# Kernel tuning notes

Measured on AMD Instinct MI355X. Metric: run time of the kernel, lower is better.

The kernel has to match this reference:

```python
import jax, jax.numpy as jnp
import numpy as np

NUM_BLOCKS, NUM_LAYERS = 3, 10
DILATIONS = tuple(2 ** l for l in range(NUM_LAYERS)) * NUM_BLOCKS  # 30 layers
B, T = 2, 8192
MEL_C, RES_C, SKIP_C, K = 80, 512, 256, 3


def conv1d(x, w, b, dilation=1):
    # x: (B, Cin, T), w: (Cout, Cin, K), 'same' padding = dilation*(K-1)//2
    pad = dilation * (w.shape[-1] - 1) // 2
    y = jax.lax.conv_general_dilated(
        x, w, window_strides=(1,), padding=[(pad, pad)],
        rhs_dilation=(dilation,), dimension_numbers=("NCH", "OIH", "NCH"))
    return y + b[None, :, None]


def setup_inputs() -> dict:
    key = jax.random.key(0)
    ks = jax.random.split(key, 16)
    s = 0.05  # keep activations in a sane range through the gated stack
    return {
        "mel_spec": jax.random.normal(ks[0], (B, MEL_C, T), jnp.float32),
        "audio":    jax.random.normal(ks[1], (B, 1, T), jnp.float32),
        "start_w":  jax.random.normal(ks[2], (RES_C, 1, 1), jnp.float32) * s,
        "start_b":  jax.random.normal(ks[3], (RES_C,), jnp.float32) * s,
        "mel_w":    jax.random.normal(ks[4], (RES_C, MEL_C, 1), jnp.float32) * s,
        "mel_b":    jax.random.normal(ks[5], (RES_C,), jnp.float32) * s,
        "dil_w":    jax.random.normal(ks[6], (30, 2 * RES_C, RES_C, K), jnp.float32) * s,
        "dil_b":    jax.random.normal(ks[7], (30, 2 * RES_C), jnp.float32) * s,
        "res_w":    jax.random.normal(ks[8], (30, RES_C, RES_C, 1), jnp.float32) * s,
        "res_b":    jax.random.normal(ks[9], (30, RES_C), jnp.float32) * s,
        "skip_w":   jax.random.normal(ks[10], (30, SKIP_C, RES_C, 1), jnp.float32) * s,
        "skip_b":   jax.random.normal(ks[11], (30, SKIP_C), jnp.float32) * s,
        "fc1_w":    jax.random.normal(ks[12], (SKIP_C, SKIP_C, 1), jnp.float32) * s,
        "fc1_b":    jax.random.normal(ks[13], (SKIP_C,), jnp.float32) * s,
        "fc2_w":    jax.random.normal(ks[14], (1, SKIP_C, 1), jnp.float32) * s,
        "fc2_b":    jax.random.normal(ks[15], (1,), jnp.float32) * s,
    }


def reference(mel_spec, audio, start_w, start_b, mel_w, mel_b,
              dil_w, dil_b, res_w, res_b, skip_w, skip_b,
              fc1_w, fc1_b, fc2_w, fc2_b):
    x = conv1d(audio, start_w, start_b)                 # (B, RES_C, T)
    mel_cond = conv1d(mel_spec, mel_w, mel_b)           # (B, RES_C, T) -- same length, no interp
    x = x + mel_cond
    skip_sum = jnp.zeros((x.shape[0], SKIP_C, x.shape[2]), x.dtype)
    for i, d in enumerate(DILATIONS):                   # 30 structurally distinct layers
        h = conv1d(x, dil_w[i], dil_b[i], dilation=d)   # (B, 2*RES_C, T)
        f, g = jnp.split(h, 2, axis=1)
        a = jnp.tanh(f) * jax.nn.sigmoid(g)             # gated activation
        x = x + conv1d(a, res_w[i], res_b[i])
        skip_sum = skip_sum + conv1d(a, skip_w[i], skip_b[i])
    y = jax.nn.relu(conv1d(skip_sum, fc1_w, fc1_b))
    return jnp.tanh(conv1d(y, fc2_w, fc2_b))            # (B, 1, T)
```

## Files before the change

### kernel.cpp

```cpp
#include <hip/hip_runtime.h>
#include <stdint.h>

#define TB 8192
#define NBATCH 2
#define RES_C 512
#define SKIP_C 256
#define MEL_C 80
#define NLAYERS 30

typedef short v8s __attribute__((ext_vector_type(8)));
typedef float v4f __attribute__((ext_vector_type(4)));
typedef unsigned short v4u16 __attribute__((ext_vector_type(4)));
typedef unsigned short v8u16 __attribute__((ext_vector_type(8)));

__device__ __forceinline__ unsigned short bf16rne(float f) {
    unsigned u = __float_as_uint(f);
    return (unsigned short)((u + 0x7fffu + ((u >> 16) & 1u)) >> 16);
}
__device__ __forceinline__ float bf2f(unsigned short h) {
    return __uint_as_float((unsigned)h << 16);
}
__device__ __forceinline__ float fsigmoid(float x) { return 1.0f / (1.0f + __expf(-x)); }
__device__ __forceinline__ float ftanh_(float x) { return 2.0f / (1.0f + __expf(-2.0f * x)) - 1.0f; }

__device__ __forceinline__ void gld16(const void* g, void* l) {
    __builtin_amdgcn_global_load_lds(
        (const __attribute__((address_space(1))) unsigned int*)g,
        (__attribute__((address_space(3))) unsigned int*)l, 16, 0, 0);
}

__global__ void k0_pack(const float* __restrict__ dil_w,
                        const float* __restrict__ res_w,
                        const float* __restrict__ skip_w,
                        unsigned short* __restrict__ WdH, unsigned short* __restrict__ WdL,
                        unsigned short* __restrict__ WrH, unsigned short* __restrict__ WrL,
                        unsigned short* __restrict__ WsH, unsigned short* __restrict__ WsL,
                        int split)
{
    const int NWd3 = NLAYERS * 1024 * 512;
    const int NWr = NLAYERS * 512 * 512;
    const int NWs = NLAYERS * 256 * 512;
    const int total = NWd3 + NWr + NWs;
    const int stride = gridDim.x * blockDim.x;
    for (int i = blockIdx.x * blockDim.x + threadIdx.x; i < total; i += stride) {
        if (i < NWd3) {
            const int ci = i & 511;
            int t2 = i >> 9;
            const int co = t2 & 1023;
            const int l = t2 >> 10;
            const float* src = dil_w + (size_t)i * 3;
            #pragma unroll
            for (int tap = 0; tap < 3; ++tap) {
                const float w = src[tap];
                const size_t d = ((size_t)(l * 3 + tap) * 1024 + co) * 512 + ci;
                const unsigned short h = bf16rne(w);
                WdH[d] = h;
                if (split) WdL[d] = bf16rne(w - bf2f(h));
            }
        } else if (i < NWd3 + NWr) {
            const int j2 = i - NWd3;
            const float w = res_w[j2];
            const unsigned short h = bf16rne(w);
            WrH[j2] = h;
            if (split) WrL[j2] = bf16rne(w - bf2f(h));
        } else {
            const int j2 = i - NWd3 - NWr;
            const float w = skip_w[j2];
            const unsigned short h = bf16rne(w);
            WsH[j2] = h;
            if (split) WsL[j2] = bf16rne(w - bf2f(h));
        }
    }
}

__global__ __launch_bounds__(512)
void k_init(const float* __restrict__ audio, const float* __restrict__ mel,
            const float* __restrict__ start_w, const float* __restrict__ start_b,
            const float* __restrict__ mel_w, const float* __restrict__ mel_b,
            float* __restrict__ x0,
            unsigned short* __restrict__ xH, unsigned short* __restrict__ xL,
            float* __restrict__ skip_acc, int split)
{
    __shared__ float smel[MEL_C][64];
    __shared__ float sa[64];
    const int tid = threadIdx.x;
    const int b = blockIdx.x >> 7;
    const int t0 = (blockIdx.x & 127) << 6;
    for (int i = tid; i < MEL_C * 64; i += 512) {
        const int m = i >> 6, tt = i & 63;
        smel[m][tt] = mel[((size_t)b * MEL_C + m) * TB + t0 + tt];
    }
    if (tid < 64) sa[tid] = audio[(size_t)b * TB + t0 + tid];
    for (int i = tid; i < 64 * SKIP_C; i += 512) {
        const int tt = i >> 8, c = i & 255;
        skip_acc[(size_t)(b * TB + t0 + tt) * SKIP_C + c] = 0.f;
    }
    __syncthreads();
    const int c = tid;
    const float sw = start_w[c];
    const float bias = start_b[c] + mel_b[c];
    const float* wrow = mel_w + (size_t)c * MEL_C;
    v4f acc[16];
    #pragma unroll
    for (int q = 0; q < 16; ++q) {
        v4f av = *(const v4f*)&sa[q * 4];
        acc[q][0] = fmaf(sw, av[0], bias);
        acc[q][1] = fmaf(sw, av[1], bias);
        acc[q][2] = fmaf(sw, av[2], bias);
        acc[q][3] = fmaf(sw, av[3], bias);
    }
    for (int m = 0; m < MEL_C; ++m) {
        const float w = wrow[m];
        #pragma unroll
        for (int q = 0; q < 16; ++q) {
            v4f mv = *(const v4f*)&smel[m][q * 4];
            acc[q][0] = fmaf(w, mv[0], acc[q][0]);
            acc[q][1] = fmaf(w, mv[1], acc[q][1]);
            acc[q][2] = fmaf(w, mv[2], acc[q][2]);
            acc[q][3] = fmaf(w, mv[3], acc[q][3]);
        }
    }
    #pragma unroll
    for (int q = 0; q < 16; ++q) {
        #pragma unroll
        for (int e = 0; e < 4; ++e) {
            const int tt = q * 4 + e;
            const size_t o = (size_t)(b * TB + t0 + tt) * RES_C + c;
            const float v = acc[q][e];
            x0[o] = v;
            const unsigned short h = bf16rne(v);
            xH[o] = h;
            if (split) xL[o] = bf16rne(v - bf2f(h));
        }
    }
}

__global__ __launch_bounds__(512)
void k1_dilgate(const unsigned short* __restrict__ xH,
                const unsigned short* __restrict__ xL,
                unsigned short* __restrict__ aH, unsigned short* __restrict__ aL,
                const unsigned short* __restrict__ WdH,
                const unsigned short* __restrict__ WdL,
                const float* __restrict__ dil_b,
                int dil, int split)
{
    __shared__ unsigned short shb2[2][128 * 128];
    __shared__ unsigned short slb2[2][128 * 128];
    const int tid = threadIdx.x;
    const int wave = tid >> 6, lane = tid & 63;
    const int quad = lane >> 4, l15 = lane & 15;
    const int p = blockIdx.x & 1;
    const int tl = blockIdx.x >> 1;
    const int b = tl >> 6;
    const int t0 = (tl & 63) << 7;
    const int fbase = p * 256 + wave * 32;
    const int srow = lane >> 4;
    const int schunk = lane & 15;

    const v4f vz = {0.f, 0.f, 0.f, 0.f};
    v4f accF[2][8], accG[2][8];
    #pragma unroll
    for (int mt = 0; mt < 2; ++mt)
        #pragma unroll
        for (int n = 0; n < 8; ++n) { accF[mt][n] = vz; accG[mt][n] = vz; }

    auto stage = [&](int chunk, int buf) {
        const int tap = chunk >> 2, ks = chunk & 3;
        const int off = (tap - 1) * dil;
        const bool allok = (t0 + off >= 0) && (t0 + 127 + off < TB);
        unsigned short* dsth = shb2[buf];
        unsigned short* dstl = slb2[buf];
        if (allok) {
            #pragma unroll
            for (int q = 0; q < 4; ++q) {
                const int rbase = wave * 16 + q * 4;
                const int r = rbase + srow;
                const size_t go = (size_t)(b * TB + t0 + r + off) * RES_C
                                + ks * 128 + ((schunk ^ (r & 7)) << 3);
                gld16(xH + go, dsth + rbase * 128);
                if (split) gld16(xL + go, dstl + rbase * 128);
            }
        } else {
            #pragma unroll
            for (int q = 0; q < 4; ++q) {
                const int rbase = wave * 16 + q * 4;
                const int r = rbase + srow;
                const int tsrc = t0 + r + off;
                const bool ok = (unsigned)tsrc < TB;
                const size_t go = (size_t)(b * TB + tsrc) * RES_C
                                + ks * 128 + ((schunk ^ (r & 7)) << 3);
                v8u16 vh = ok ? *(const v8u16*)(xH + go) : (v8u16)0;
                *(v8u16*)(dsth + rbase * 128 + (lane << 3)) = vh;
                if (split) {
                    v8u16 vl = ok ? *(const v8u16*)(xL + go) : (v8u16)0;
                    *(v8u16*)(dstl + rbase * 128 + (lane << 3)) = vl;
                }
            }
        }
    };

    auto compute = [&](int chunk, int buf) {
        const int tap = chunk >> 2, ks = chunk & 3;
        const unsigned short* WHT = WdH + (size_t)tap * 1024 * 512;
        const unsigned short* WLT = WdL + (size_t)tap * 1024 * 512;
        const unsigned short* shb = shb2[buf];
        const unsigned short* slb = slb2[buf];
        #pragma unroll
        for (int kc = 0; kc < 4; ++kc) {
            const int kg = ks * 128 + kc * 32 + quad * 8;
            v8s afh[2], agh[2], afl[2], agl[2];
            #pragma unroll
            for (int mt = 0; mt < 2; ++mt) {
                const int row = fbase + mt * 16 + l15;
                afh[mt] = *(const v8s*)(WHT + (size_t)row * 512 + kg);
                agh[mt] = *(const v8s*)(WHT + (size_t)(row + 512) * 512 + kg);
                if (split) {
                    afl[mt] = *(const v8s*)(WLT + (size_t)row * 512 + kg);
                    agl[mt] = *(const v8s*)(WLT + (size_t)(row + 512) * 512 + kg);
                }
            }
            const int nsw = ((kc * 4 + quad) ^ (l15 & 7)) << 3;
            #pragma unroll
            for (int nh = 0; nh < 2; ++nh) {
                v8s bh[4], bl[4];
                #pragma unroll
                for (int j = 0; j < 4; ++j) {
                    const int trow = (nh * 4 + j) * 16 + l15;
                    bh[j] = *(const v8s*)(shb + trow * 128 + nsw);
                    if (split) bl[j] = *(const v8s*)(slb + trow * 128 + nsw);
                }
                #pragma unroll
                for (int mt = 0; mt < 2; ++mt)
                    #pragma unroll
                    for (int j = 0; j < 4; ++j) {
                        const int n = nh * 4 + j;
                        accF[mt][n] = __builtin_amdgcn_mfma_f32_16x16x32_bf16(
                            afh[mt], bh[j], accF[mt][n], 0, 0, 0);
                        accG[mt][n] = __builtin_amdgcn_mfma_f32_16x16x32_bf16(
                            agh[mt], bh[j], accG[mt][n], 0, 0, 0);
                        if (split) {
                            accF[mt][n] = __builtin_amdgcn_mfma_f32_16x16x32_bf16(
                                afh[mt], bl[j], accF[mt][n], 0, 0, 0);
                            accF[mt][n] = __builtin_amdgcn_mfma_f32_16x16x32_bf16(
                                afl[mt], bh[j], accF[mt][n], 0, 0, 0);
                            accG[mt][n] = __builtin_amdgcn_mfma_f32_16x16x32_bf16(
                                agh[mt], bl[j], accG[mt][n], 0, 0, 0);
                            accG[mt][n] = __builtin_amdgcn_mfma_f32_16x16x32_bf16(
                                agl[mt], bh[j], accG[mt][n], 0, 0, 0);
                        }
                    }
            }
        }
    };

    stage(0, 0);
    __syncthreads();
    for (int chunk = 0; chunk < 12; ++chunk) {
        if (chunk < 11) stage(chunk + 1, (chunk + 1) & 1);
        compute(chunk, chunk & 1);
        __syncthreads();
    }

    unsigned short* aHb = aH + (size_t)b * TB * RES_C;
    unsigned short* aLb = aL + (size_t)b * TB * RES_C;
    #pragma unroll
    for (int mt = 0; mt < 2; ++mt) {
        const int ch = p * 256 + wave * 32 + mt * 16 + quad * 4;
        const float4 bF = *(const float4*)(dil_b + ch);
        const float4 bG = *(const float4*)(dil_b + 512 + ch);
        #pragma unroll
        for (int n = 0; n < 8; ++n) {
            const int t = t0 + n * 16 + l15;
            float a0 = ftanh_(accF[mt][n][0] + bF.x) * fsigmoid(accG[mt][n][0] + bG.x);
            float a1 = ftanh_(accF[mt][n][1] + bF.y) * fsigmoid(accG[mt][n][1] + bG.y);
            float a2 = ftanh_(accF[mt][n][2] + bF.z) * fsigmoid(accG[mt][n][2] + bG.z);
            float a3 = ftanh_(accF[mt][n][3] + bF.w) * fsigmoid(accG[mt][n][3] + bG.w);
            v4u16 oh;
            oh[0] = bf16rne(a0); oh[1] = bf16rne(a1);
            oh[2] = bf16rne(a2); oh[3] = bf16rne(a3);
            *(v4u16*)(aHb + (size_t)t * RES_C + ch) = oh;
            if (split) {
                v4u16 ol;
                ol[0] = bf16rne(a0 - bf2f(oh[0]));
                ol[1] = bf16rne(a1 - bf2f(oh[1]));
                ol[2] = bf16rne(a2 - bf2f(oh[2]));
                ol[3] = bf16rne(a3 - bf2f(oh[3]));
                *(v4u16*)(aLb + (size_t)t * RES_C + ch) = ol;
            }
        }
    }
}

__global__ __launch_bounds__(512)
void k3_resskip(float* __restrict__ x,
                unsigned short* __restrict__ xH, unsigned short* __restrict__ xL,
                float* __restrict__ skip_acc,
                const unsigned short* __restrict__ aH,
                const unsigned short* __restrict__ aL,
                const unsigned short* __restrict__ WrH, const unsigned short* __restrict__ WrL,
                const unsigned short* __restrict__ WsH, const unsigned short* __restrict__ WsL,
                const float* __restrict__ res_b, const float* __restrict__ skip_b,
                int split)
{
    __shared__ unsigned short shi[32 * 512];
    __shared__ unsigned short slo[32 * 512];
    const int tid = threadIdx.x;
    const int wave = tid >> 6, lane = tid & 63;
    const int quad = lane >> 4, l15 = lane & 15;
    const int b = blockIdx.x >> 8;
    const int t0 = (blockIdx.x & 255) << 5;
    {
        #pragma unroll
        for (int q = 0; q < 4; ++q) {
            const int r = wave * 4 + q;
            const size_t go = (size_t)(b * TB + t0 + r) * RES_C + ((lane ^ (r & 7)) << 3);
            gld16(aH + go, shi + r * 512);
            if (split) gld16(aL + go, slo + r * 512);
        }
    }
    __syncthreads();
    const v4f vz = {0.f, 0.f, 0.f, 0.f};
    v4f acc[6][2];
    #pragma unroll
    for (int i = 0; i < 6; ++i) { acc[i][0] = vz; acc[i][1] = vz; }

    for (int kc = 0; kc < 16; ++kc) {
        const int k0 = kc * 32 + quad * 8;
        const int nsw = ((kc * 4 + quad) ^ (l15 & 7)) << 3;
        v8s bh[2], bl[2];
        #pragma unroll
        for (int j = 0; j < 2; ++j) {
            bh[j] = *(const v8s*)(shi + (j * 16 + l15) * 512 + nsw);
            if (split) bl[j] = *(const v8s*)(slo + (j * 16 + l15) * 512 + nsw);
        }
        #pragma unroll
        for (int i = 0; i < 6; ++i) {
            const int row = (wave * 6 + i) * 16 + l15;
            v8s ah, al;
            if (row < 512) {
                ah = *(const v8s*)(WrH + (size_t)row * 512 + k0);
                if (split) al = *(const v8s*)(WrL + (size_t)row * 512 + k0);
            } else {
                ah = *(const v8s*)(WsH + (size_t)(row - 512) * 512 + k0);
                if (split) al = *(const v8s*)(WsL + (size_t)(row - 512) * 512 + k0);
            }
            #pragma unroll
            for (int j = 0; j < 2; ++j) {
                acc[i][j] = __builtin_amdgcn_mfma_f32_16x16x32_bf16(ah, bh[j], acc[i][j], 0, 0, 0);
                if (split) {
                    acc[i][j] = __builtin_amdgcn_mfma_f32_16x16x32_bf16(ah, bl[j], acc[i][j], 0, 0, 0);
                    acc[i][j] = __builtin_amdgcn_mfma_f32_16x16x32_bf16(al, bh[j], acc[i][j], 0, 0, 0);
                }
            }
        }
    }
    #pragma unroll
    for (int i = 0; i < 6; ++i) {
        const int rb = (wave * 6 + i) * 16 + quad * 4;
        if (rb < 512) {
            const float4 bias = *(const float4*)(res_b + rb);
            #pragma unroll
            for (int j = 0; j < 2; ++j) {
                const int t = t0 + j * 16 + l15;
                const size_t o = (size_t)(b * TB + t) * RES_C + rb;
                float4 v = *(const float4*)(x + o);
                v.x += acc[i][j][0] + bias.x;
                v.y += acc[i][j][1] + bias.y;
                v.z += acc[i][j][2] + bias.z;
                v.w += acc[i][j][3] + bias.w;
                *(float4*)(x + o) = v;
                v4u16 oh;
                oh[0] = bf16rne(v.x); oh[1] = bf16rne(v.y);
                oh[2] = bf16rne(v.z); oh[3] = bf16rne(v.w);
                *(v4u16*)(xH + o) = oh;
                if (split) {
                    v4u16 ol;
                    ol[0] = bf16rne(v.x - bf2f(oh[0]));
                    ol[1] = bf16rne(v.y - bf2f(oh[1]));
                    ol[2] = bf16rne(v.z - bf2f(oh[2]));
                    ol[3] = bf16rne(v.w - bf2f(oh[3]));
                    *(v4u16*)(xL + o) = ol;
                }
            }
        } else {
            const int rs = rb - 512;
            const float4 bias = *(const float4*)(skip_b + rs);
            #pragma unroll
            for (int j = 0; j < 2; ++j) {
                const int t = t0 + j * 16 + l15;
                const size_t o = (size_t)(b * TB + t) * SKIP_C + rs;
                float4 v = *(const float4*)(skip_acc + o);
                v.x += acc[i][j][0] + bias.x;
                v.y += acc[i][j][1] + bias.y;
                v.z += acc[i][j][2] + bias.z;
                v.w += acc[i][j][3] + bias.w;
                *(float4*)(skip_acc + o) = v;
            }
        }
    }
}

__global__ __launch_bounds__(256)
void k4_final(const float* __restrict__ skip_acc,
              const float* __restrict__ fc1_w, const float* __restrict__ fc1_b,
              const float* __restrict__ fc2_w, const float* __restrict__ fc2_b,
              float* __restrict__ out)
{
    __shared__ float stile[32 * 260];
    __shared__ float part[8][32];
    const int tid = threadIdx.x;
    const int b = blockIdx.x >> 8;
    const int t0 = (blockIdx.x & 255) << 5;
    {
        const int r = tid >> 3, sub = tid & 7;
        const float* srow = skip_acc + (size_t)(b * TB + t0 + r) * SKIP_C;
        float* drow = stile + r * 260;
        #pragma unroll
        for (int i = 0; i < 8; ++i) {
            const int c = (i * 8 + sub) * 4;
            *(float4*)(drow + c) = *(const float4*)(srow + c);
        }
    }
    __syncthreads();
    const int t = tid & 31;
    const int w = tid >> 5;
    float y[32];
    #pragma unroll
    for (int co = 0; co < 32; ++co) y[co] = fc1_b[w * 32 + co];
    const float* srow = stile + t * 260;
    for (int ci = 0; ci < SKIP_C; ++ci) {
        const float s = srow[ci];
        const float* wcol = fc1_w + (size_t)(w * 32) * SKIP_C + ci;
        #pragma unroll
        for (int co = 0; co < 32; ++co)
            y[co] = fmaf(wcol[(size_t)co * SKIP_C], s, y[co]);
    }
    float partial = 0.f;
    #pragma unroll
    for (int co = 0; co < 32; ++co) {
        const float v = y[co] > 0.f ? y[co] : 0.f;
        partial = fmaf(fc2_w[w * 32 + co], v, partial);
    }
    part[w][t] = partial;
    __syncthreads();
    if (tid < 32) {
        float v = fc2_b[0];
        #pragma unroll
        for (int k = 0; k < 8; ++k) v += part[k][tid];
        out[(size_t)b * TB + t0 + tid] = ftanh_(v);
    }
}

extern "C" void kernel_launch(void* const* d_in, const int* in_sizes, int n_in,
                              void* d_out, int out_size, void* d_ws, size_t ws_size,
                              hipStream_t stream)
{
    const float* mel     = (const float*)d_in[0];
    const float* audio   = (const float*)d_in[1];
    const float* start_w = (const float*)d_in[2];
    const float* start_b = (const float*)d_in[3];
    const float* mel_w   = (const float*)d_in[4];
    const float* mel_b   = (const float*)d_in[5];
    const float* dil_b   = (const float*)d_in[7];
    const float* res_b   = (const float*)d_in[9];
    const float* skip_b  = (const float*)d_in[11];
    const float* fc1_w   = (const float*)d_in[12];
    const float* fc1_b   = (const float*)d_in[13];
    const float* fc2_w   = (const float*)d_in[14];
    const float* fc2_b   = (const float*)d_in[15];
    float* out = (float*)d_out;

    char* ws = (char*)d_ws;
    const size_t szWd = (size_t)NLAYERS * 3 * 1024 * 512 * 2;
    const size_t szWr = (size_t)NLAYERS * 512 * 512 * 2;
    const size_t szWs = (size_t)NLAYERS * 256 * 512 * 2;
    const size_t szX32 = (size_t)NBATCH * TB * RES_C * 4;
    const size_t szX16 = (size_t)NBATCH * TB * RES_C * 2;
    const size_t szSk = (size_t)NBATCH * TB * SKIP_C * 4;
    size_t off = 0;
    unsigned short* WdH = (unsigned short*)(ws + off); off += szWd;
    unsigned short* WrH = (unsigned short*)(ws + off); off += szWr;
    unsigned short* WsH = (unsigned short*)(ws + off); off += szWs;
    float* x = (float*)(ws + off); off += szX32;
    unsigned short* xH = (unsigned short*)(ws + off); off += szX16;
    unsigned short* aH = (unsigned short*)(ws + off); off += szX16;
    float* skip_acc = (float*)(ws + off); off += szSk;
    const size_t lo_need = szX16 * 2 + szWd + szWr + szWs;
    const int split = (off + lo_need <= ws_size) ? 1 : 0;
    unsigned short* xL = split ? (unsigned short*)(ws + off) : xH; if (split) off += szX16;
    unsigned short* aL = split ? (unsigned short*)(ws + off) : aH; if (split) off += szX16;
    unsigned short* WdL = split ? (unsigned short*)(ws + off) : WdH; if (split) off += szWd;
    unsigned short* WrL = split ? (unsigned short*)(ws + off) : WrH; if (split) off += szWr;
    unsigned short* WsL = split ? (unsigned short*)(ws + off) : WsH; if (split) off += szWs;

    k0_pack<<<8192, 256, 0, stream>>>((const float*)d_in[6], (const float*)d_in[8],
                                      (const float*)d_in[10],
                                      WdH, WdL, WrH, WrL, WsH, WsL, split);
    k_init<<<NBATCH * (TB / 64), 512, 0, stream>>>(
        audio, mel, start_w, start_b, mel_w, mel_b, x, xH, xL, skip_acc, split);

    for (int l = 0; l < NLAYERS; ++l) {
        const int dil = 1 << (l % 10);
        k1_dilgate<<<256, 512, 0, stream>>>(xH, xL, aH, aL,
            WdH + (size_t)l * 3 * 1024 * 512, WdL + (size_t)l * 3 * 1024 * 512,
            dil_b + (size_t)l * 1024, dil, split);
        k3_resskip<<<512, 512, 0, stream>>>(x, xH, xL, skip_acc, aH, aL,
            WrH + (size_t)l * 512 * 512, WrL + (size_t)l * 512 * 512,
            WsH + (size_t)l * 256 * 512, WsL + (size_t)l * 256 * 512,
            res_b + (size_t)l * 512, skip_b + (size_t)l * 256, split);
    }
    k4_final<<<512, 256, 0, stream>>>(skip_acc, fc1_w, fc1_b, fc2_w, fc2_b, out);
}
```

Before: 8.376 ms.

## Halve dilated-conv time tile and remap blocks across XCDs

```diff
diff --git a/kernel.cpp b/kernel.cpp
--- a/kernel.cpp
+++ b/kernel.cpp
@@ -144,36 +144,39 @@
                 const float* __restrict__ dil_b,
                 int dil, int split)
 {
-    __shared__ unsigned short shb2[2][128 * 128];
-    __shared__ unsigned short slb2[2][128 * 128];
+    __shared__ unsigned short shb2[2][64 * 128];
+    __shared__ unsigned short slb2[2][64 * 128];
     const int tid = threadIdx.x;
     const int wave = tid >> 6, lane = tid & 63;
     const int quad = lane >> 4, l15 = lane & 15;
-    const int p = blockIdx.x & 1;
-    const int tl = blockIdx.x >> 1;
-    const int b = tl >> 6;
-    const int t0 = (tl & 63) << 7;
+    const int idx = blockIdx.x;
+    const int xcd = idx & 7;
+    const int j64 = idx >> 3;
+    const int p = xcd & 1;
+    const int tl = (xcd >> 1) * 64 + j64;
+    const int b = tl >> 7;
+    const int t0 = (tl & 127) << 6;
     const int fbase = p * 256 + wave * 32;
     const int srow = lane >> 4;
     const int schunk = lane & 15;
 
     const v4f vz = {0.f, 0.f, 0.f, 0.f};
-    v4f accF[2][8], accG[2][8];
+    v4f accF[2][4], accG[2][4];
     #pragma unroll
     for (int mt = 0; mt < 2; ++mt)
         #pragma unroll
-        for (int n = 0; n < 8; ++n) { accF[mt][n] = vz; accG[mt][n] = vz; }
+        for (int n = 0; n < 4; ++n) { accF[mt][n] = vz; accG[mt][n] = vz; }
 
     auto stage = [&](int chunk, int buf) {
         const int tap = chunk >> 2, ks = chunk & 3;
         const int off = (tap - 1) * dil;
-        const bool allok = (t0 + off >= 0) && (t0 + 127 + off < TB);
+        const bool allok = (t0 + off >= 0) && (t0 + 63 + off < TB);
         unsigned short* dsth = shb2[buf];
         unsigned short* dstl = slb2[buf];
         if (allok) {
             #pragma unroll
-            for (int q = 0; q < 4; ++q) {
-                const int rbase = wave * 16 + q * 4;
+            for (int q = 0; q < 2; ++q) {
+                const int rbase = wave * 8 + q * 4;
                 const int r = rbase + srow;
                 const size_t go = (size_t)(b * TB + t0 + r + off) * RES_C
                                 + ks * 128 + ((schunk ^ (r & 7)) << 3);
@@ -182,8 +185,8 @@
             }
         } else {
             #pragma unroll
-            for (int q = 0; q < 4; ++q) {
-                const int rbase = wave * 16 + q * 4;
+            for (int q = 0; q < 2; ++q) {
+                const int rbase = wave * 8 + q * 4;
                 const int r = rbase + srow;
                 const int tsrc = t0 + r + off;
                 const bool ok = (unsigned)tsrc < TB;
@@ -220,36 +223,32 @@
                 }
             }
             const int nsw = ((kc * 4 + quad) ^ (l15 & 7)) << 3;
-            #pragma unroll
-            for (int nh = 0; nh < 2; ++nh) {
-                v8s bh[4], bl[4];
+            v8s bh[4], bl[4];
+            #pragma unroll
+            for (int j = 0; j < 4; ++j) {
+                const int trow = j * 16 + l15;
+                bh[j] = *(const v8s*)(shb + trow * 128 + nsw);
+                if (split) bl[j] = *(const v8s*)(slb + trow * 128 + nsw);
+            }
+            #pragma unroll
+            for (int mt = 0; mt < 2; ++mt)
                 #pragma unroll
                 for (int j = 0; j < 4; ++j) {
-                    const int trow = (nh * 4 + j) * 16 + l15;
-                    bh[j] = *(const v8s*)(shb + trow * 128 + nsw);
-                    if (split) bl[j] = *(const v8s*)(slb + trow * 128 + nsw);
+                    accF[mt][j] = __builtin_amdgcn_mfma_f32_16x16x32_bf16(
+                        afh[mt], bh[j], accF[mt][j], 0, 0, 0);
+                    accG[mt][j] = __builtin_amdgcn_mfma_f32_16x16x32_bf16(
+                        agh[mt], bh[j], accG[mt][j], 0, 0, 0);
+                    if (split) {
+                        accF[mt][j] = __builtin_amdgcn_mfma_f32_16x16x32_bf16(
+                            afh[mt], bl[j], accF[mt][j], 0, 0, 0);
+                        accF[mt][j] = __builtin_amdgcn_mfma_f32_16x16x32_bf16(
+                            afl[mt], bh[j], accF[mt][j], 0, 0, 0);
+                        accG[mt][j] = __builtin_amdgcn_mfma_f32_16x16x32_bf16(
+                            agh[mt], bl[j], accG[mt][j], 0, 0, 0);
+                        accG[mt][j] = __builtin_amdgcn_mfma_f32_16x16x32_bf16(
+                            agl[mt], bh[j], accG[mt][j], 0, 0, 0);
+                    }
                 }
-                #pragma unroll
-                for (int mt = 0; mt < 2; ++mt)
-                    #pragma unroll
-                    for (int j = 0; j < 4; ++j) {
-                        const int n = nh * 4 + j;
-                        accF[mt][n] = __builtin_amdgcn_mfma_f32_16x16x32_bf16(
-                            afh[mt], bh[j], accF[mt][n], 0, 0, 0);
-                        accG[mt][n] = __builtin_amdgcn_mfma_f32_16x16x32_bf16(
-                            agh[mt], bh[j], accG[mt][n], 0, 0, 0);
-                        if (split) {
-                            accF[mt][n] = __builtin_amdgcn_mfma_f32_16x16x32_bf16(
-                                afh[mt], bl[j], accF[mt][n], 0, 0, 0);
-                            accF[mt][n] = __builtin_amdgcn_mfma_f32_16x16x32_bf16(
-                                afl[mt], bh[j], accF[mt][n], 0, 0, 0);
-                            accG[mt][n] = __builtin_amdgcn_mfma_f32_16x16x32_bf16(
-                                agh[mt], bl[j], accG[mt][n], 0, 0, 0);
-                            accG[mt][n] = __builtin_amdgcn_mfma_f32_16x16x32_bf16(
-                                agl[mt], bh[j], accG[mt][n], 0, 0, 0);
-                        }
-                    }
-            }
         }
     };
 
@@ -269,7 +268,7 @@
         const float4 bF = *(const float4*)(dil_b + ch);
         const float4 bG = *(const float4*)(dil_b + 512 + ch);
         #pragma unroll
-        for (int n = 0; n < 8; ++n) {
+        for (int n = 0; n < 4; ++n) {
             const int t = t0 + n * 16 + l15;
             float a0 = ftanh_(accF[mt][n][0] + bF.x) * fsigmoid(accG[mt][n][0] + bG.x);
             float a1 = ftanh_(accF[mt][n][1] + bF.y) * fsigmoid(accG[mt][n][1] + bG.y);
@@ -501,7 +500,7 @@
 
     for (int l = 0; l < NLAYERS; ++l) {
         const int dil = 1 << (l % 10);
-        k1_dilgate<<<256, 512, 0, stream>>>(xH, xL, aH, aL,
+        k1_dilgate<<<512, 512, 0, stream>>>(xH, xL, aH, aL,
             WdH + (size_t)l * 3 * 1024 * 512, WdL + (size_t)l * 3 * 1024 * 512,
             dil_b + (size_t)l * 1024, dil, split);
         k3_resskip<<<512, 512, 0, stream>>>(x, xH, xL, skip_acc, aH, aL,
```

Measured after the change: 10.78 ms. 28.7% more time.

## Pre-pack weights into per-wave MFMA fragment order with interleaved hi/lo

Applied to the files above, without the earlier changes.

```diff
diff --git a/kernel.cpp b/kernel.cpp
--- a/kernel.cpp
+++ b/kernel.cpp
@@ -32,11 +32,11 @@
 __global__ void k0_pack(const float* __restrict__ dil_w,
                         const float* __restrict__ res_w,
                         const float* __restrict__ skip_w,
-                        unsigned short* __restrict__ WdH, unsigned short* __restrict__ WdL,
-                        unsigned short* __restrict__ WrH, unsigned short* __restrict__ WrL,
-                        unsigned short* __restrict__ WsH, unsigned short* __restrict__ WsL,
+                        unsigned short* __restrict__ Wp,
+                        unsigned short* __restrict__ Wq,
                         int split)
 {
+    const int TC = split + 1;
     const int NWd3 = NLAYERS * 1024 * 512;
     const int NWr = NLAYERS * 512 * 512;
     const int NWs = NLAYERS * 256 * 512;
@@ -48,27 +48,44 @@
             int t2 = i >> 9;
             const int co = t2 & 1023;
             const int l = t2 >> 10;
+            const int fg = co >> 9, r = co & 511;
+            const int p = r >> 8, wv = (r >> 5) & 7, mt = (r >> 4) & 1, l15 = r & 15;
+            const int ks = ci >> 7, kc = (ci >> 5) & 3, quad = (ci >> 3) & 3, e = ci & 7;
+            const int lane = quad * 16 + l15;
             const float* src = dil_w + (size_t)i * 3;
+            unsigned short* lbase = Wp + (size_t)l * 3072 * TC * 512;
             #pragma unroll
             for (int tap = 0; tap < 3; ++tap) {
                 const float w = src[tap];
-                const size_t d = ((size_t)(l * 3 + tap) * 1024 + co) * 512 + ci;
+                const int idx = ((p * 8 + wv) * 192
+                               + ((tap * 4 + ks) * 16 + kc * 4 + mt * 2 + fg)) * TC;
+                unsigned short* d = lbase + (size_t)idx * 512 + lane * 8 + e;
                 const unsigned short h = bf16rne(w);
-                WdH[d] = h;
-                if (split) WdL[d] = bf16rne(w - bf2f(h));
-            }
-        } else if (i < NWd3 + NWr) {
-            const int j2 = i - NWd3;
-            const float w = res_w[j2];
+                d[0] = h;
+                if (split) d[512] = bf16rne(w - bf2f(h));
+            }
+        } else {
+            int rowc, ci, l;
+            float w;
+            if (i < NWd3 + NWr) {
+                const int j2 = i - NWd3;
+                l = j2 >> 18; rowc = (j2 >> 9) & 511; ci = j2 & 511;
+                w = res_w[j2];
+            } else {
+                const int j2 = i - NWd3 - NWr;
+                l = j2 >> 17; rowc = ((j2 >> 9) & 255) + 512; ci = j2 & 511;
+                w = skip_w[j2];
+            }
+            const int rowgrp = rowc >> 4, l15 = rowc & 15;
+            const int wv = rowgrp / 6, i6 = rowgrp % 6;
+            const int kc = ci >> 5, quad = (ci >> 3) & 3, e = ci & 7;
+            const int lane = quad * 16 + l15;
+            const int idx = (wv * 96 + kc * 6 + i6) * TC;
+            unsigned short* d = Wq + (size_t)l * 768 * TC * 512 + (size_t)idx * 512
+                              + lane * 8 + e;
             const unsigned short h = bf16rne(w);
-            WrH[j2] = h;
-            if (split) WrL[j2] = bf16rne(w - bf2f(h));
-        } else {
-            const int j2 = i - NWd3 - NWr;
-            const float w = skip_w[j2];
-            const unsigned short h = bf16rne(w);
-            WsH[j2] = h;
-            if (split) WsL[j2] = bf16rne(w - bf2f(h));
+            d[0] = h;
+            if (split) d[512] = bf16rne(w - bf2f(h));
         }
     }
 }
@@ -139,13 +156,13 @@
 void k1_dilgate(const unsigned short* __restrict__ xH,
                 const unsigned short* __restrict__ xL,
                 unsigned short* __restrict__ aH, unsigned short* __restrict__ aL,
-                const unsigned short* __restrict__ WdH,
-                const unsigned short* __restrict__ WdL,
+                const unsigned short* __restrict__ Wp,
                 const float* __restrict__ dil_b,
                 int dil, int split)
 {
     __shared__ unsigned short shb2[2][128 * 128];
     __shared__ unsigned short slb2[2][128 * 128];
+    const int TC = split + 1;
     const int tid = threadIdx.x;
     const int wave = tid >> 6, lane = tid & 63;
     const int quad = lane >> 4, l15 = lane & 15;
@@ -153,9 +170,9 @@
     const int tl = blockIdx.x >> 1;
     const int b = tl >> 6;
     const int t0 = (tl & 63) << 7;
-    const int fbase = p * 256 + wave * 32;
     const int srow = lane >> 4;
     const int schunk = lane & 15;
+    const unsigned short* wpw = Wp + ((size_t)(p * 8 + wave) * 192 * TC) * 512 + lane * 8;
 
     const v4f vz = {0.f, 0.f, 0.f, 0.f};
     v4f accF[2][8], accG[2][8];
@@ -201,22 +218,20 @@
 
     auto compute = [&](int chunk, int buf) {
         const int tap = chunk >> 2, ks = chunk & 3;
-        const unsigned short* WHT = WdH + (size_t)tap * 1024 * 512;
-        const unsigned short* WLT = WdL + (size_t)tap * 1024 * 512;
+        const unsigned short* cb = wpw + (size_t)((tap * 4 + ks) * 16) * TC * 512;
         const unsigned short* shb = shb2[buf];
         const unsigned short* slb = slb2[buf];
         #pragma unroll
         for (int kc = 0; kc < 4; ++kc) {
-            const int kg = ks * 128 + kc * 32 + quad * 8;
+            const unsigned short* ck = cb + (size_t)(kc * 4) * TC * 512;
             v8s afh[2], agh[2], afl[2], agl[2];
             #pragma unroll
             for (int mt = 0; mt < 2; ++mt) {
-                const int row = fbase + mt * 16 + l15;
-                afh[mt] = *(const v8s*)(WHT + (size_t)row * 512 + kg);
-                agh[mt] = *(const v8s*)(WHT + (size_t)(row + 512) * 512 + kg);
+                afh[mt] = *(const v8s*)(ck + (size_t)((mt * 2 + 0) * TC) * 512);
+                agh[mt] = *(const v8s*)(ck + (size_t)((mt * 2 + 1) * TC) * 512);
                 if (split) {
-                    afl[mt] = *(const v8s*)(WLT + (size_t)row * 512 + kg);
-                    agl[mt] = *(const v8s*)(WLT + (size_t)(row + 512) * 512 + kg);
+                    afl[mt] = *(const v8s*)(ck + (size_t)((mt * 2 + 0) * TC + 1) * 512);
+                    agl[mt] = *(const v8s*)(ck + (size_t)((mt * 2 + 1) * TC + 1) * 512);
                 }
             }
             const int nsw = ((kc * 4 + quad) ^ (l15 & 7)) << 3;
@@ -297,18 +312,19 @@
                 float* __restrict__ skip_acc,
                 const unsigned short* __restrict__ aH,
                 const unsigned short* __restrict__ aL,
-                const unsigned short* __restrict__ WrH, const unsigned short* __restrict__ WrL,
-                const unsigned short* __restrict__ WsH, const unsigned short* __restrict__ WsL,
+                const unsigned short* __restrict__ Wq,
                 const float* __restrict__ res_b, const float* __restrict__ skip_b,
                 int split)
 {
     __shared__ unsigned short shi[32 * 512];
     __shared__ unsigned short slo[32 * 512];
+    const int TC = split + 1;
     const int tid = threadIdx.x;
     const int wave = tid >> 6, lane = tid & 63;
     const int quad = lane >> 4, l15 = lane & 15;
     const int b = blockIdx.x >> 8;
     const int t0 = (blockIdx.x & 255) << 5;
+    const unsigned short* wqw = Wq + (size_t)wave * 96 * TC * 512 + lane * 8;
     {
         #pragma unroll
         for (int q = 0; q < 4; ++q) {
@@ -325,7 +341,6 @@
     for (int i = 0; i < 6; ++i) { acc[i][0] = vz; acc[i][1] = vz; }
 
     for (int kc = 0; kc < 16; ++kc) {
-        const int k0 = kc * 32 + quad * 8;
         const int nsw = ((kc * 4 + quad) ^ (l15 & 7)) << 3;
         v8s bh[2], bl[2];
         #pragma unroll
@@ -335,15 +350,10 @@
         }
         #pragma unroll
         for (int i = 0; i < 6; ++i) {
-            const int row = (wave * 6 + i) * 16 + l15;
+            const unsigned short* ck = wqw + (size_t)((kc * 6 + i) * TC) * 512;
             v8s ah, al;
-            if (row < 512) {
-                ah = *(const v8s*)(WrH + (size_t)row * 512 + k0);
-                if (split) al = *(const v8s*)(WrL + (size_t)row * 512 + k0);
-            } else {
-                ah = *(const v8s*)(WsH + (size_t)(row - 512) * 512 + k0);
-                if (split) al = *(const v8s*)(WsL + (size_t)(row - 512) * 512 + k0);
-            }
+            ah = *(const v8s*)(ck);
+            if (split) al = *(const v8s*)(ck + 512);
             #pragma unroll
             for (int j = 0; j < 2; ++j) {
                 acc[i][j] = __builtin_amdgcn_mfma_f32_16x16x32_bf16(ah, bh[j], acc[i][j], 0, 0, 0);
@@ -471,42 +481,38 @@
     float* out = (float*)d_out;
 
     char* ws = (char*)d_ws;
-    const size_t szWd = (size_t)NLAYERS * 3 * 1024 * 512 * 2;
-    const size_t szWr = (size_t)NLAYERS * 512 * 512 * 2;
-    const size_t szWs = (size_t)NLAYERS * 256 * 512 * 2;
     const size_t szX32 = (size_t)NBATCH * TB * RES_C * 4;
     const size_t szX16 = (size_t)NBATCH * TB * RES_C * 2;
     const size_t szSk = (size_t)NBATCH * TB * SKIP_C * 4;
+    const size_t need2 = (size_t)NLAYERS * 3072 * 2 * 512 * 2
+                       + (size_t)NLAYERS * 768 * 2 * 512 * 2
+                       + szX32 + szSk + 4 * szX16;
+    const int split = (ws_size >= need2) ? 1 : 0;
+    const int TC = split + 1;
+    const size_t szWp = (size_t)NLAYERS * 3072 * TC * 512 * 2;
+    const size_t szWq = (size_t)NLAYERS * 768 * TC * 512 * 2;
     size_t off = 0;
-    unsigned short* WdH = (unsigned short*)(ws + off); off += szWd;
-    unsigned short* WrH = (unsigned short*)(ws + off); off += szWr;
-    unsigned short* WsH = (unsigned short*)(ws + off); off += szWs;
+    unsigned short* Wp = (unsigned short*)(ws + off); off += szWp;
+    unsigned short* Wq = (unsigned short*)(ws + off); off += szWq;
     float* x = (float*)(ws + off); off += szX32;
     unsigned short* xH = (unsigned short*)(ws + off); off += szX16;
     unsigned short* aH = (unsigned short*)(ws + off); off += szX16;
     float* skip_acc = (float*)(ws + off); off += szSk;
-    const size_t lo_need = szX16 * 2 + szWd + szWr + szWs;
-    const int split = (off + lo_need <= ws_size) ? 1 : 0;
     unsigned short* xL = split ? (unsigned short*)(ws + off) : xH; if (split) off += szX16;
     unsigned short* aL = split ? (unsigned short*)(ws + off) : aH; if (split) off += szX16;
-    unsigned short* WdL = split ? (unsigned short*)(ws + off) : WdH; if (split) off += szWd;
-    unsigned short* WrL = split ? (unsigned short*)(ws + off) : WrH; if (split) off += szWr;
-    unsigned short* WsL = split ? (unsigned short*)(ws + off) : WsH; if (split) off += szWs;
 
     k0_pack<<<8192, 256, 0, stream>>>((const float*)d_in[6], (const float*)d_in[8],
-                                      (const float*)d_in[10],
-                                      WdH, WdL, WrH, WrL, WsH, WsL, split);
+                                      (const float*)d_in[10], Wp, Wq, split);
     k_init<<<NBATCH * (TB / 64), 512, 0, stream>>>(
         audio, mel, start_w, start_b, mel_w, mel_b, x, xH, xL, skip_acc, split);
 
     for (int l = 0; l < NLAYERS; ++l) {
         const int dil = 1 << (l % 10);
         k1_dilgate<<<256, 512, 0, stream>>>(xH, xL, aH, aL,
-            WdH + (size_t)l * 3 * 1024 * 512, WdL + (size_t)l * 3 * 1024 * 512,
+            Wp + (size_t)l * 3072 * TC * 512,
             dil_b + (size_t)l * 1024, dil, split);
         k3_resskip<<<512, 512, 0, stream>>>(x, xH, xL, skip_acc, aH, aL,
-            WrH + (size_t)l * 512 * 512, WrL + (size_t)l * 512 * 512,
-            WsH + (size_t)l * 256 * 512, WsL + (size_t)l * 256 * 512,
+            Wq + (size_t)l * 768 * TC * 512,
             res_b + (size_t)l * 512, skip_b + (size_t)l * 256, split);
     }
     k4_final<<<512, 256, 0, stream>>>(skip_acc, fc1_w, fc1_b, fc2_w, fc2_b, out);
```

Result: faster. 7.253 ms (-13.4%).
